# Kernel tuning notes

Hardware: AMD Instinct MI355X
Metric: run time of the kernel (lower is better)

## Reference

```python
import jax, jax.numpy as jnp
import numpy as np

B, L, H = 2, 2048, 1024
N_HEADS = 16
HEAD = H // N_HEADS
LN_EPS = 1e-12


def setup_inputs() -> dict:
    key = jax.random.key(0)
    ks = jax.random.split(key, 8)
    s = 1.0 / np.sqrt(H)
    return {
        "embeddings": jax.random.normal(ks[0], (B, L, H), dtype=jnp.float32),
        "mask": jnp.zeros((B, 1, 1, L), dtype=jnp.float32),
        "Wq": jax.random.normal(ks[1], (H, H), dtype=jnp.float32) * s,
        "bq": jnp.zeros((H,), dtype=jnp.float32),
        "Wk": jax.random.normal(ks[2], (H, H), dtype=jnp.float32) * s,
        "bk": jnp.zeros((H,), dtype=jnp.float32),
        "Wv": jax.random.normal(ks[3], (H, H), dtype=jnp.float32) * s,
        "bv": jnp.zeros((H,), dtype=jnp.float32),
        "Wo": jax.random.normal(ks[4], (H, H), dtype=jnp.float32) * s,
        "bo": jnp.zeros((H,), dtype=jnp.float32),
        "ln_gamma": jnp.ones((H,), dtype=jnp.float32),
        "ln_beta": jnp.zeros((H,), dtype=jnp.float32),
    }


def _layer_norm(x, gamma, beta):
    mu = jnp.mean(x, axis=-1, keepdims=True)
    var = jnp.mean(jnp.square(x - mu), axis=-1, keepdims=True)
    return (x - mu) * jax.lax.rsqrt(var + LN_EPS) * gamma + beta


def reference(embeddings, mask, Wq, bq, Wk, bk, Wv, bv, Wo, bo, ln_gamma, ln_beta):
    b, l, h = embeddings.shape
    # QKV projections, split heads -> [b, n_heads, l, head]
    def split_heads(x):
        return x.reshape(b, l, N_HEADS, HEAD).transpose(0, 2, 1, 3)
    q = split_heads(embeddings @ Wq + bq)
    k = split_heads(embeddings @ Wk + bk)
    v = split_heads(embeddings @ Wv + bv)
    # Faithful to source: energies use Q @ V^T, scaled by sqrt(n_heads)
    energies = jnp.einsum("bhqd,bhkd->bhqk", q, v) / np.sqrt(N_HEADS) + mask
    weights = jax.nn.softmax(energies, axis=3)
    # Faithful to source: attended = weights @ K
    attended = jnp.einsum("bhqk,bhkd->bhqd", weights, k)
    attended = attended.transpose(0, 2, 1, 3).reshape(b, l, h)
    # Residual feed-forward (BertSelfOutput style): dense + residual + LN
    out = attended @ Wo + bo
    return _layer_norm(out + embeddings, ln_gamma, ln_beta)
```

## Files before the change

kernel.cpp:

```cpp
#include <hip/hip_runtime.h>

#define LOG2E 1.44269504f
#define C_QSCALE 0.360673760f
#define C_SHIFT  34.6246810f
typedef unsigned short u16;
typedef short bf16x8 __attribute__((ext_vector_type(8)));
typedef float f32x4 __attribute__((ext_vector_type(4)));
typedef unsigned short u16x4 __attribute__((ext_vector_type(4)));
typedef unsigned int u32x4 __attribute__((ext_vector_type(4)));

#define BB 2
#define LL 2048
#define HH 1024
#define NH 16
#define HD 64
#define ML (BB*LL)

__device__ __forceinline__ u16 f2bf(float f) {
  union { float f; unsigned u; } v; v.f = f;
  unsigned r = v.u + 0x7FFFu + ((v.u >> 16) & 1u);
  return (u16)(r >> 16);
}
__device__ __forceinline__ u16 f2bf_trunc(float f) {
  union { float f; unsigned u; } v; v.f = f;
  return (u16)(v.u >> 16);
}
__device__ __forceinline__ float bf2f(u16 u) {
  union { unsigned u; float f; } v; v.u = ((unsigned)u) << 16;
  return v.f;
}
__device__ __forceinline__ void gload_lds16(const u16* g, u16* l) {
  __builtin_amdgcn_global_load_lds((const __attribute__((address_space(1))) void*)g,
                                   (__attribute__((address_space(3))) void*)l, 16, 0, 0);
}
__device__ __forceinline__ unsigned cvt_pk_bf16(float lo, float hi) {
  unsigned r;
  asm("v_cvt_pk_bf16_f32 %0, %1, %2" : "=v"(r) : "v"(lo), "v"(hi));
  return r;
}
__device__ __forceinline__ void pl16swap(unsigned &a, unsigned &b) {
  asm("v_permlane16_swap_b32 %0, %1" : "+v"(a), "+v"(b));
}
__device__ __forceinline__ void pl32swap(unsigned &a, unsigned &b) {
  asm("v_permlane32_swap_b32 %0, %1" : "+v"(a), "+v"(b));
}

__global__ __launch_bounds__(256) void k_prep(const float* __restrict__ E, u16* __restrict__ X,
                                              const float* W0, const float* W1,
                                              const float* W2, const float* W3,
                                              u16* __restrict__ WT) {
  __shared__ __align__(16) u16 T[64*72];
  if (blockIdx.x < 2048) {
    int idx = (blockIdx.x * 256 + threadIdx.x) * 8;
    float4 a = *(const float4*)(E + idx);
    float4 b = *(const float4*)(E + idx + 4);
    bf16x8 o;
    o[0]=f2bf(a.x); o[1]=f2bf(a.y); o[2]=f2bf(a.z); o[3]=f2bf(a.w);
    o[4]=f2bf(b.x); o[5]=f2bf(b.y); o[6]=f2bf(b.z); o[7]=f2bf(b.w);
    *(bf16x8*)(X + idx) = o;
    return;
  }
  int bz = blockIdx.x - 2048;
  int z = bz >> 8, rem = bz & 255, bx = rem & 15, by = rem >> 4;
  const float* W = (z==0)?W0:(z==1)?W1:(z==2)?W2:W3;
  u16* dst = WT + (size_t)z * HH * HH;
  int t = threadIdx.x;
  int n0 = bx * 64, k0 = by * 64;
  int kl = t >> 2, nc = t & 3;
  #pragma unroll
  for (int u = 0; u < 4; ++u) {
    float4 v = *(const float4*)(W + (size_t)(k0 + kl) * HH + n0 + nc*16 + u*4);
    int nb = nc*16 + u*4;
    T[(nb+0)*72 + kl] = f2bf(v.x);
    T[(nb+1)*72 + kl] = f2bf(v.y);
    T[(nb+2)*72 + kl] = f2bf(v.z);
    T[(nb+3)*72 + kl] = f2bf(v.w);
  }
  __syncthreads();
  int nl = t >> 2, kc = (t & 3) * 16;
  #pragma unroll
  for (int e = 0; e < 2; ++e) {
    bf16x8 v = *(const bf16x8*)(T + nl*72 + kc + e*8);
    *(bf16x8*)(dst + (size_t)(n0+nl)*HH + k0 + kc + e*8) = v;
  }
}

__global__ __launch_bounds__(256) void k_gemm(const u16* __restrict__ A, const u16* __restrict__ Bt,
                                              const float* __restrict__ b0, const float* __restrict__ b1,
                                              const float* __restrict__ b2,
                                              u16* __restrict__ QH, u16* __restrict__ KV) {
  __shared__ __align__(16) u16 As[2][128*32];
  __shared__ __align__(16) u16 Bs[2][128*32];
  int tid = threadIdx.x;
  int lane = tid & 63, w = tid >> 6;
  int c = lane & 15, g = lane >> 4;
  int bn0 = blockIdx.x * 128, bm0 = blockIdx.y * 128;
  int wm0 = (w >> 1) * 64, wn0 = (w & 1) * 64;
  int z = bn0 >> 10;
  bool swapd = (z != 1);
  const u16* srcA = swapd ? Bt : A;
  const u16* srcB = swapd ? A : Bt;
  int baseA = swapd ? bn0 : bm0;
  int baseB = swapd ? bm0 : bn0;

  f32x4 acc[4][4];
  #pragma unroll
  for (int mt = 0; mt < 4; ++mt)
    #pragma unroll
    for (int nt = 0; nt < 4; ++nt)
      acc[mt][nt] = (f32x4){0.f,0.f,0.f,0.f};

  #pragma unroll
  for (int it = 0; it < 2; ++it) {
    int ch = tid + it*256, row = ch >> 2, col = (ch & 3) * 8;
    gload_lds16(srcA + (size_t)(baseA + row) * HH + col, &As[0][ch*8]);
    gload_lds16(srcB + (size_t)(baseB + row) * HH + col, &Bs[0][ch*8]);
  }
  for (int kt = 0; kt < 32; ++kt) {
    __syncthreads();
    int cb = kt & 1;
    if (kt < 31) {
      int k0 = (kt + 1) * 32, nb = (kt + 1) & 1;
      #pragma unroll
      for (int it = 0; it < 2; ++it) {
        int ch = tid + it*256, row = ch >> 2, col = (ch & 3) * 8;
        gload_lds16(srcA + (size_t)(baseA + row) * HH + k0 + col, &As[nb][ch*8]);
        gload_lds16(srcB + (size_t)(baseB + row) * HH + k0 + col, &Bs[nb][ch*8]);
      }
    }
    bf16x8 af[4], bfr[4];
    #pragma unroll
    for (int i = 0; i < 4; ++i) {
      af[i]  = *(const bf16x8*)(&As[cb][0] + (wm0 + i*16 + c)*32 + g*8);
      bfr[i] = *(const bf16x8*)(&Bs[cb][0] + (wn0 + i*16 + c)*32 + g*8);
    }
    #pragma unroll
    for (int mt = 0; mt < 4; ++mt)
      #pragma unroll
      for (int nt = 0; nt < 4; ++nt)
        acc[mt][nt] = __builtin_amdgcn_mfma_f32_16x16x32_bf16(af[mt], bfr[nt], acc[mt][nt], 0, 0, 0);
  }

  if (z == 1) {
    #pragma unroll
    for (int nt = 0; nt < 4; ++nt) {
      int n = bn0 + wn0 + nt*16 + c;
      int nn = n & 1023, h = nn >> 6, d = nn & 63;
      float bv = b1[nn];
      #pragma unroll
      for (int mt = 0; mt < 4; ++mt) {
        int m0 = bm0 + wm0 + mt*16 + 4*g;
        int b = m0 >> 11, keyl = m0 & 2047;
        int tt = keyl >> 6, chunk = (keyl >> 3) & 7, s = keyl & 7;
        u16x4 pk;
        #pragma unroll
        for (int r = 0; r < 4; ++r) pk[r] = f2bf(acc[mt][nt][r] + bv);
        *(u16x4*)(KV + ((size_t)((b*NH + h)*32 + tt))*8192 + d*64 + ((chunk ^ (d & 7))*8) + s) = pk;
      }
    }
  } else {
    #pragma unroll
    for (int mt = 0; mt < 4; ++mt) {
      int nidx0 = bn0 + wm0 + mt*16 + 4*g;
      int nn0 = nidx0 & 1023, h = nn0 >> 6, d0 = nn0 & 63;
      const float* bp = (z == 0) ? b0 : b2;
      float4 bv = *(const float4*)(bp + nn0);
      #pragma unroll
      for (int nt = 0; nt < 4; ++nt) {
        int tok = bm0 + wn0 + nt*16 + c;
        int b = tok >> 11, l = tok & 2047;
        u16x4 o;
        o[0] = f2bf(acc[mt][nt][0] + bv.x);
        o[1] = f2bf(acc[mt][nt][1] + bv.y);
        o[2] = f2bf(acc[mt][nt][2] + bv.z);
        o[3] = f2bf(acc[mt][nt][3] + bv.w);
        if (z == 0) {
          *(u16x4*)(QH + (((size_t)(b*NH + h)) * LL + l) * HD + d0) = o;
        } else {
          int tt = l >> 6;
          *(u16x4*)(KV + ((size_t)((b*NH + h)*32 + tt))*8192 + 4096
                    + (l & 63)*64 + (((d0 >> 3) ^ (l & 7))*8) + (d0 & 7)) = o;
        }
      }
    }
  }
}

__global__ __launch_bounds__(256) void k_gemm_o(const u16* __restrict__ ATT, const u16* __restrict__ Wt,
                                                const float* __restrict__ bias,
                                                float* __restrict__ outf) {
  __shared__ __align__(16) u16 As[2][128*32];
  __shared__ __align__(16) u16 Bs[2][64*32];
  int tid = threadIdx.x;
  int lane = tid & 63, w = tid >> 6;
  int c = lane & 15, g = lane >> 4;
  int bn0 = blockIdx.x * 128, bm0 = blockIdx.y * 64;
  int wm0 = (w >> 1) * 64, wn0 = (w & 1) * 32;

  f32x4 acc[4][2];
  #pragma unroll
  for (int mt = 0; mt < 4; ++mt)
    #pragma unroll
    for (int nt = 0; nt < 2; ++nt)
      acc[mt][nt] = (f32x4){0.f,0.f,0.f,0.f};

  #pragma unroll
  for (int it = 0; it < 2; ++it) {
    int ch = tid + it*256, row = ch >> 2, col = (ch & 3) * 8;
    gload_lds16(Wt + (size_t)(bn0 + row) * HH + col, &As[0][ch*8]);
  }
  { int row = tid >> 2, col = (tid & 3) * 8;
    gload_lds16(ATT + (size_t)(bm0 + row) * HH + col, &Bs[0][tid*8]); }

  for (int kt = 0; kt < 32; ++kt) {
    __syncthreads();
    int cb = kt & 1;
    if (kt < 31) {
      int k0 = (kt + 1) * 32, nb = (kt + 1) & 1;
      #pragma unroll
      for (int it = 0; it < 2; ++it) {
        int ch = tid + it*256, row = ch >> 2, col = (ch & 3) * 8;
        gload_lds16(Wt + (size_t)(bn0 + row) * HH + k0 + col, &As[nb][ch*8]);
      }
      int row = tid >> 2, col = (tid & 3) * 8;
      gload_lds16(ATT + (size_t)(bm0 + row) * HH + k0 + col, &Bs[nb][tid*8]);
    }
    bf16x8 af[4], bfr[2];
    #pragma unroll
    for (int i = 0; i < 4; ++i)
      af[i] = *(const bf16x8*)(&As[cb][0] + (wm0 + i*16 + c)*32 + g*8);
    #pragma unroll
    for (int j = 0; j < 2; ++j)
      bfr[j] = *(const bf16x8*)(&Bs[cb][0] + (wn0 + j*16 + c)*32 + g*8);
    #pragma unroll
    for (int mt = 0; mt < 4; ++mt)
      #pragma unroll
      for (int nt = 0; nt < 2; ++nt)
        acc[mt][nt] = __builtin_amdgcn_mfma_f32_16x16x32_bf16(af[mt], bfr[nt], acc[mt][nt], 0, 0, 0);
  }
  #pragma unroll
  for (int mt = 0; mt < 4; ++mt) {
    int n0 = bn0 + wm0 + mt*16 + 4*g;
    float4 bv = *(const float4*)(bias + n0);
    #pragma unroll
    for (int nt = 0; nt < 2; ++nt) {
      int tok = bm0 + wn0 + nt*16 + c;
      float4 o;
      o.x = acc[mt][nt][0] + bv.x;
      o.y = acc[mt][nt][1] + bv.y;
      o.z = acc[mt][nt][2] + bv.z;
      o.w = acc[mt][nt][3] + bv.w;
      *(float4*)(outf + (size_t)tok * HH + n0) = o;
    }
  }
}

__global__ __launch_bounds__(256, 4) void k_attn(const u16* __restrict__ QH, const u16* __restrict__ KV,
                                              const float* __restrict__ mask,
                                              u16* __restrict__ PO0, u16* __restrict__ PO1,
                                              float* __restrict__ PL) {
  __shared__ __align__(16) u16 sKV[2][8192];
  int tid = threadIdx.x;
  int lane = tid & 63, w = tid >> 6;
  int c = lane & 15, g = lane >> 4;
  int phys = blockIdx.x + (blockIdx.y << 4) + (blockIdx.z << 5);
  int virt = (phys & 7) * 128 + (phys >> 3);
  int bx = virt & 15;
  int z = (virt >> 4) & 1;
  int bh = virt >> 5, b = bh >> 4;
  int q0 = bx * 128 + w * 32;
  size_t qbase = (size_t)bh * LL * HD;
  const u16* kvg = KV + (size_t)bh * 32 * 8192 + (size_t)z * 16 * 8192;
  const float* mptr = mask + b * LL + z * 1024;

  bf16x8 aq[2][2];
  #pragma unroll
  for (int qi = 0; qi < 2; ++qi)
    #pragma unroll
    for (int ks = 0; ks < 2; ++ks)
      aq[qi][ks] = *(const bf16x8*)(QH + qbase + (size_t)(q0 + qi*16 + c) * HD + ks*32 + g*8);

  bf16x8 ones;
  #pragma unroll
  for (int i = 0; i < 8; ++i) ones[i] = (short)0x3F80;

  f32x4 O[2][4], lac[2];
  #pragma unroll
  for (int qi = 0; qi < 2; ++qi) {
    lac[qi] = (f32x4){0.f,0.f,0.f,0.f};
    #pragma unroll
    for (int dt = 0; dt < 4; ++dt) O[qi][dt] = (f32x4){0.f,0.f,0.f,0.f};
  }

  #pragma unroll
  for (int it = 0; it < 4; ++it) {
    int i = (tid + it*256) * 8;
    gload_lds16(kvg + i, &sKV[0][0] + i);
  }

  for (int tt = 0; tt < 16; ++tt) {
    __syncthreads();
    int cb = tt & 1;
    if (tt < 15) {
      #pragma unroll
      for (int it = 0; it < 4; ++it) {
        int i = (tid + it*256) * 8;
        gload_lds16(kvg + (size_t)(tt+1)*8192 + i, &sKV[cb^1][0] + i);
      }
    }
    const u16* kvp = &sKV[cb][0];
    int kv0 = tt * 64;

    unsigned X[2][4][2];
    #pragma unroll
    for (int nt = 0; nt < 4; ++nt) {
      int vrow = nt*16 + c;
      bf16x8 vb0 = *(const bf16x8*)(kvp + 4096 + vrow*64 + ((g ^ (c & 7))*8));
      bf16x8 vb1 = *(const bf16x8*)(kvp + 4096 + vrow*64 + (((4 + g) ^ (c & 7))*8));
      float4 mv = *(const float4*)(mptr + kv0 + nt*16 + 4*g);
      float mt0 = fmaf(mv.x, LOG2E, -C_SHIFT);
      float mt1 = fmaf(mv.y, LOG2E, -C_SHIFT);
      float mt2 = fmaf(mv.z, LOG2E, -C_SHIFT);
      float mt3 = fmaf(mv.w, LOG2E, -C_SHIFT);
      #pragma unroll
      for (int qi = 0; qi < 2; ++qi) {
        f32x4 sa = (f32x4){0.f,0.f,0.f,0.f};
        sa = __builtin_amdgcn_mfma_f32_16x16x32_bf16(vb0, aq[qi][0], sa, 0,0,0);
        sa = __builtin_amdgcn_mfma_f32_16x16x32_bf16(vb1, aq[qi][1], sa, 0,0,0);
        float p0 = exp2f(fmaf(sa[0], C_QSCALE, mt0));
        float p1 = exp2f(fmaf(sa[1], C_QSCALE, mt1));
        float p2 = exp2f(fmaf(sa[2], C_QSCALE, mt2));
        float p3 = exp2f(fmaf(sa[3], C_QSCALE, mt3));
        X[qi][nt][0] = cvt_pk_bf16(p0, p1);
        X[qi][nt][1] = cvt_pk_bf16(p2, p3);
      }
    }
    bf16x8 ap[2][2];
    #pragma unroll
    for (int qi = 0; qi < 2; ++qi) {
      #pragma unroll
      for (int h = 0; h < 2; ++h) {
        unsigned x0 = X[qi][2*h][0],   x1 = X[qi][2*h][1];
        unsigned x2 = X[qi][2*h+1][0], x3 = X[qi][2*h+1][1];
        pl32swap(x0, x2); pl16swap(x0, x2);
        pl32swap(x1, x3); pl16swap(x1, x3);
        union { u32x4 u; bf16x8 b; } cvt;
        cvt.u[0] = x0; cvt.u[1] = x1; cvt.u[2] = x2; cvt.u[3] = x3;
        ap[qi][h] = cvt.b;
        lac[qi] = __builtin_amdgcn_mfma_f32_16x16x32_bf16(ones, ap[qi][h], lac[qi], 0,0,0);
      }
    }
    #pragma unroll
    for (int dt = 0; dt < 4; ++dt) {
      int d = dt*16 + c;
      bf16x8 bk0 = *(const bf16x8*)(kvp + d*64 + ((g ^ (c & 7))*8));
      bf16x8 bk1 = *(const bf16x8*)(kvp + d*64 + (((4 + g) ^ (c & 7))*8));
      #pragma unroll
      for (int qi = 0; qi < 2; ++qi) {
        O[qi][dt] = __builtin_amdgcn_mfma_f32_16x16x32_bf16(bk0, ap[qi][0], O[qi][dt], 0,0,0);
        O[qi][dt] = __builtin_amdgcn_mfma_f32_16x16x32_bf16(bk1, ap[qi][1], O[qi][dt], 0,0,0);
      }
    }
  }
  u16* POp = (z == 0) ? PO0 : PO1;
  #pragma unroll
  for (int qi = 0; qi < 2; ++qi) {
    int q = q0 + qi*16 + c;
    size_t qrow = (size_t)bh * LL + q;
    if (g == 0) PL[(size_t)(z*32 + bh) * LL + q] = lac[qi][0];
    #pragma unroll
    for (int dt = 0; dt < 4; ++dt) {
      u16x4 o;
      #pragma unroll
      for (int r = 0; r < 4; ++r) o[r] = f2bf(O[qi][dt][r]);
      *(u16x4*)(POp + qrow*HD + dt*16 + 4*g) = o;
    }
  }
}

__global__ __launch_bounds__(256) void k_combine(const u16* __restrict__ PO0,
                                                 const u16* __restrict__ PO1,
                                                 const float* __restrict__ PL,
                                                 u16* __restrict__ ATT) {
  int bh = blockIdx.y, b = bh >> 4, h = bh & 15;
  int q = blockIdx.x * 128 + (threadIdx.x >> 1);
  int dh = (threadIdx.x & 1) * 32;
  size_t r0 = ((size_t)bh * LL + q) * HD + dh;
  float inv = 1.0f / (PL[(size_t)bh * LL + q] + PL[(size_t)(32 + bh) * LL + q]);
  u16* dst = ATT + ((size_t)(b*LL + q)) * HH + h*HD + dh;
  #pragma unroll
  for (int e = 0; e < 4; ++e) {
    bf16x8 a0 = *(const bf16x8*)(PO0 + r0 + e*8);
    bf16x8 a1 = *(const bf16x8*)(PO1 + r0 + e*8);
    bf16x8 o;
    #pragma unroll
    for (int i = 0; i < 8; ++i)
      o[i] = (short)f2bf((bf2f((u16)a0[i]) + bf2f((u16)a1[i])) * inv);
    *(bf16x8*)(dst + e*8) = o;
  }
}

__global__ __launch_bounds__(256) void k_ln(const float* __restrict__ OF, const float* __restrict__ E,
                                            const float* __restrict__ gamma, const float* __restrict__ beta,
                                            float* __restrict__ out) {
  int row = blockIdx.x;
  int tid = threadIdx.x, lane = tid & 63, w = tid >> 6;
  size_t basei = (size_t)row * HH + tid*4;
  float4 a = *(const float4*)(OF + basei);
  float4 e = *(const float4*)(E + basei);
  float x0 = a.x + e.x, x1 = a.y + e.y, x2 = a.z + e.z, x3 = a.w + e.w;
  float s1 = x0+x1+x2+x3;
  float s2 = x0*x0+x1*x1+x2*x2+x3*x3;
  #pragma unroll
  for (int off = 32; off; off >>= 1) { s1 += __shfl_xor(s1, off); s2 += __shfl_xor(s2, off); }
  __shared__ float r1[4], r2[4];
  if (lane == 0) { r1[w] = s1; r2[w] = s2; }
  __syncthreads();
  s1 = r1[0]+r1[1]+r1[2]+r1[3];
  s2 = r2[0]+r2[1]+r2[2]+r2[3];
  float mu = s1 * (1.0f/HH);
  float var = s2 * (1.0f/HH) - mu*mu;
  float rs = rsqrtf(fmaxf(var, 0.f) + 1e-12f);
  int colb = tid*4;
  float4 gm = *(const float4*)(gamma + colb);
  float4 bt = *(const float4*)(beta + colb);
  float4 o;
  o.x = (x0-mu)*rs*gm.x + bt.x;
  o.y = (x1-mu)*rs*gm.y + bt.y;
  o.z = (x2-mu)*rs*gm.z + bt.z;
  o.w = (x3-mu)*rs*gm.w + bt.w;
  *(float4*)(out + basei) = o;
}

extern "C" void kernel_launch(void* const* d_in, const int* in_sizes, int n_in,
                              void* d_out, int out_size, void* d_ws, size_t ws_size,
                              hipStream_t stream) {
  const float* E    = (const float*)d_in[0];
  const float* mask = (const float*)d_in[1];
  const float* Wq   = (const float*)d_in[2];
  const float* bq   = (const float*)d_in[3];
  const float* Wk   = (const float*)d_in[4];
  const float* bk   = (const float*)d_in[5];
  const float* Wv   = (const float*)d_in[6];
  const float* bv   = (const float*)d_in[7];
  const float* Wo   = (const float*)d_in[8];
  const float* bo   = (const float*)d_in[9];
  const float* gam  = (const float*)d_in[10];
  const float* bet  = (const float*)d_in[11];

  const size_t MH = (size_t)ML * HH;
  u16* XBF = (u16*)d_ws;
  u16* WT  = XBF + MH;
  u16* QH  = WT + 4*(size_t)HH*HH;
  u16* KV  = QH + MH;
  u16* ATT = KV + 2*MH;
  u16* PO0 = ATT + MH;
  u16* PO1 = PO0 + MH;
  float* out = (float*)d_out;
  float* PL = out;
  float* OF = (float*)PO0;

  k_prep<<<dim3(3072), 256, 0, stream>>>(E, XBF, Wq, Wk, Wv, Wo, WT);
  k_gemm<<<dim3(24,32), 256, 0, stream>>>(XBF, WT, bq, bk, bv, QH, KV);
  k_attn<<<dim3(16,2,32), 256, 0, stream>>>(QH, KV, mask, PO0, PO1, PL);
  k_combine<<<dim3(16,32), 256, 0, stream>>>(PO0, PO1, PL, ATT);
  k_gemm_o<<<dim3(8,64), 256, 0, stream>>>(ATT, WT + 3*(size_t)HH*HH, bo, OF);
  k_ln<<<dim3(ML), 256, 0, stream>>>(OF, E, gam, bet, out);
}
```

Measured before the change: 235.8 us.

## Software-pipeline attention: overlap next-tile QV scores with current PV accumulation

Result: slower. 257.5 us (+9.2%).

```diff
diff --git a/kernel.cpp b/kernel.cpp
--- a/kernel.cpp
+++ b/kernel.cpp
@@ -21,10 +21,6 @@
   unsigned r = v.u + 0x7FFFu + ((v.u >> 16) & 1u);
   return (u16)(r >> 16);
 }
-__device__ __forceinline__ u16 f2bf_trunc(float f) {
-  union { float f; unsigned u; } v; v.f = f;
-  return (u16)(v.u >> 16);
-}
 __device__ __forceinline__ float bf2f(u16 u) {
   union { unsigned u; float f; } v; v.u = ((unsigned)u) << 16;
   return v.f;
@@ -32,6 +28,9 @@
 __device__ __forceinline__ void gload_lds16(const u16* g, u16* l) {
   __builtin_amdgcn_global_load_lds((const __attribute__((address_space(1))) void*)g,
                                    (__attribute__((address_space(3))) void*)l, 16, 0, 0);
+}
+__device__ __forceinline__ float fast_exp2(float x) {
+  float r; asm("v_exp_f32 %0, %1" : "=v"(r) : "v"(x)); return r;
 }
 __device__ __forceinline__ unsigned cvt_pk_bf16(float lo, float hi) {
   unsigned r;
@@ -259,7 +258,8 @@
                                               const float* __restrict__ mask,
                                               u16* __restrict__ PO0, u16* __restrict__ PO1,
                                               float* __restrict__ PL) {
-  __shared__ __align__(16) u16 sKV[2][8192];
+  __shared__ __align__(16) u16 sK[3*4096];
+  __shared__ __align__(16) u16 sV[2*4096];
   int tid = threadIdx.x;
   int lane = tid & 63, w = tid >> 6;
   int c = lane & 15, g = lane >> 4;
@@ -292,76 +292,97 @@
     for (int dt = 0; dt < 4; ++dt) O[qi][dt] = (f32x4){0.f,0.f,0.f,0.f};
   }
 
-  #pragma unroll
-  for (int it = 0; it < 4; ++it) {
-    int i = (tid + it*256) * 8;
-    gload_lds16(kvg + i, &sKV[0][0] + i);
-  }
-
-  for (int tt = 0; tt < 16; ++tt) {
-    __syncthreads();
-    int cb = tt & 1;
-    if (tt < 15) {
-      #pragma unroll
-      for (int it = 0; it < 4; ++it) {
-        int i = (tid + it*256) * 8;
-        gload_lds16(kvg + (size_t)(tt+1)*8192 + i, &sKV[cb^1][0] + i);
-      }
-    }
-    const u16* kvp = &sKV[cb][0];
-    int kv0 = tt * 64;
-
-    unsigned X[2][4][2];
+  int i0 = tid * 8, i1 = (tid + 256) * 8;
+
+  auto dma_tile = [&](int t, int koff, int voff) {
+    const u16* src = kvg + (size_t)t * 8192;
+    gload_lds16(src + i0,        sK + koff + i0);
+    gload_lds16(src + i1,        sK + koff + i1);
+    gload_lds16(src + 4096 + i0, sV + voff + i0);
+    gload_lds16(src + 4096 + i1, sV + voff + i1);
+  };
+
+  auto s_phase = [&](int t, int voff, bf16x8 (&apn)[2][2]) {
+    const u16* vr = sV + voff;
+    int kv0 = t * 64;
+    float mt[4][4];
     #pragma unroll
     for (int nt = 0; nt < 4; ++nt) {
-      int vrow = nt*16 + c;
-      bf16x8 vb0 = *(const bf16x8*)(kvp + 4096 + vrow*64 + ((g ^ (c & 7))*8));
-      bf16x8 vb1 = *(const bf16x8*)(kvp + 4096 + vrow*64 + (((4 + g) ^ (c & 7))*8));
       float4 mv = *(const float4*)(mptr + kv0 + nt*16 + 4*g);
-      float mt0 = fmaf(mv.x, LOG2E, -C_SHIFT);
-      float mt1 = fmaf(mv.y, LOG2E, -C_SHIFT);
-      float mt2 = fmaf(mv.z, LOG2E, -C_SHIFT);
-      float mt3 = fmaf(mv.w, LOG2E, -C_SHIFT);
-      #pragma unroll
-      for (int qi = 0; qi < 2; ++qi) {
+      mt[nt][0] = fmaf(mv.x, LOG2E, -C_SHIFT);
+      mt[nt][1] = fmaf(mv.y, LOG2E, -C_SHIFT);
+      mt[nt][2] = fmaf(mv.z, LOG2E, -C_SHIFT);
+      mt[nt][3] = fmaf(mv.w, LOG2E, -C_SHIFT);
+    }
+    #pragma unroll
+    for (int qi = 0; qi < 2; ++qi) {
+      unsigned X[4][2];
+      #pragma unroll
+      for (int nt = 0; nt < 4; ++nt) {
+        int vrow = nt*16 + c;
+        bf16x8 vb0 = *(const bf16x8*)(vr + vrow*64 + ((g ^ (c & 7))*8));
+        bf16x8 vb1 = *(const bf16x8*)(vr + vrow*64 + (((4 + g) ^ (c & 7))*8));
         f32x4 sa = (f32x4){0.f,0.f,0.f,0.f};
         sa = __builtin_amdgcn_mfma_f32_16x16x32_bf16(vb0, aq[qi][0], sa, 0,0,0);
         sa = __builtin_amdgcn_mfma_f32_16x16x32_bf16(vb1, aq[qi][1], sa, 0,0,0);
-        float p0 = exp2f(fmaf(sa[0], C_QSCALE, mt0));
-        float p1 = exp2f(fmaf(sa[1], C_QSCALE, mt1));
-        float p2 = exp2f(fmaf(sa[2], C_QSCALE, mt2));
-        float p3 = exp2f(fmaf(sa[3], C_QSCALE, mt3));
-        X[qi][nt][0] = cvt_pk_bf16(p0, p1);
-        X[qi][nt][1] = cvt_pk_bf16(p2, p3);
-      }
-    }
-    bf16x8 ap[2][2];
-    #pragma unroll
-    for (int qi = 0; qi < 2; ++qi) {
+        float p0 = fast_exp2(fmaf(sa[0], C_QSCALE, mt[nt][0]));
+        float p1 = fast_exp2(fmaf(sa[1], C_QSCALE, mt[nt][1]));
+        float p2 = fast_exp2(fmaf(sa[2], C_QSCALE, mt[nt][2]));
+        float p3 = fast_exp2(fmaf(sa[3], C_QSCALE, mt[nt][3]));
+        X[nt][0] = cvt_pk_bf16(p0, p1);
+        X[nt][1] = cvt_pk_bf16(p2, p3);
+      }
       #pragma unroll
       for (int h = 0; h < 2; ++h) {
-        unsigned x0 = X[qi][2*h][0],   x1 = X[qi][2*h][1];
-        unsigned x2 = X[qi][2*h+1][0], x3 = X[qi][2*h+1][1];
+        unsigned x0 = X[2*h][0],   x1 = X[2*h][1];
+        unsigned x2 = X[2*h+1][0], x3 = X[2*h+1][1];
         pl32swap(x0, x2); pl16swap(x0, x2);
         pl32swap(x1, x3); pl16swap(x1, x3);
-        union { u32x4 u; bf16x8 b; } cvt;
+        union { u32x4 u; bf16x8 bv; } cvt;
         cvt.u[0] = x0; cvt.u[1] = x1; cvt.u[2] = x2; cvt.u[3] = x3;
-        ap[qi][h] = cvt.b;
-        lac[qi] = __builtin_amdgcn_mfma_f32_16x16x32_bf16(ones, ap[qi][h], lac[qi], 0,0,0);
-      }
-    }
+        apn[qi][h] = cvt.bv;
+        lac[qi] = __builtin_amdgcn_mfma_f32_16x16x32_bf16(ones, apn[qi][h], lac[qi], 0,0,0);
+      }
+    }
+  };
+
+  auto pv_phase = [&](int koff, bf16x8 (&apc)[2][2]) {
+    const u16* kr = sK + koff;
     #pragma unroll
     for (int dt = 0; dt < 4; ++dt) {
       int d = dt*16 + c;
-      bf16x8 bk0 = *(const bf16x8*)(kvp + d*64 + ((g ^ (c & 7))*8));
-      bf16x8 bk1 = *(const bf16x8*)(kvp + d*64 + (((4 + g) ^ (c & 7))*8));
+      bf16x8 bk0 = *(const bf16x8*)(kr + d*64 + ((g ^ (c & 7))*8));
+      bf16x8 bk1 = *(const bf16x8*)(kr + d*64 + (((4 + g) ^ (c & 7))*8));
       #pragma unroll
       for (int qi = 0; qi < 2; ++qi) {
-        O[qi][dt] = __builtin_amdgcn_mfma_f32_16x16x32_bf16(bk0, ap[qi][0], O[qi][dt], 0,0,0);
-        O[qi][dt] = __builtin_amdgcn_mfma_f32_16x16x32_bf16(bk1, ap[qi][1], O[qi][dt], 0,0,0);
-      }
-    }
-  }
+        O[qi][dt] = __builtin_amdgcn_mfma_f32_16x16x32_bf16(bk0, apc[qi][0], O[qi][dt], 0,0,0);
+        O[qi][dt] = __builtin_amdgcn_mfma_f32_16x16x32_bf16(bk1, apc[qi][1], O[qi][dt], 0,0,0);
+      }
+    }
+  };
+
+  bf16x8 apA[2][2], apB[2][2];
+  int kr_ = 0, kn_ = 4096, kw_ = 8192;
+
+  dma_tile(0, 0, 0);
+  __syncthreads();
+  dma_tile(1, 4096, 4096);
+  s_phase(0, 0, apA);
+
+  #pragma unroll 2
+  for (int j = 0; j < 16; ++j) {
+    __syncthreads();
+    if (j < 14) dma_tile(j + 2, kw_, (j & 1) * 4096);
+    if (j & 1) {
+      if (j < 15) s_phase(j + 1, ((j + 1) & 1) * 4096, apA);
+      pv_phase(kr_, apB);
+    } else {
+      if (j < 15) s_phase(j + 1, ((j + 1) & 1) * 4096, apB);
+      pv_phase(kr_, apA);
+    }
+    int t_ = kr_; kr_ = kn_; kn_ = kw_; kw_ = t_;
+  }
+
   u16* POp = (z == 0) ? PO0 : PO1;
   #pragma unroll
   for (int qi = 0; qi < 2; ++qi) {
```
